# Kernel tuning notes

Measured on AMD Instinct MI355X. Metric: run time of the kernel, lower is better.

The kernel has to match this reference:

```python
import jax, jax.numpy as jnp
import numpy as np

EMBED_DIM = 1024
NUM_HEADS = 16
HEAD_DIM = EMBED_DIM // NUM_HEADS


def setup_inputs() -> dict:
    key = jax.random.key(0)
    ks = jax.random.split(key, 9)
    s = 1.0 / np.sqrt(EMBED_DIM)
    inp = {"x": jax.random.normal(ks[0], (2, 2048, EMBED_DIM), dtype=jnp.float32)}
    for i, name in enumerate(["q", "k", "v", "out"]):
        inp[f"W_{name}"] = jax.random.uniform(ks[1 + 2 * i], (EMBED_DIM, EMBED_DIM), jnp.float32, -s, s)
        inp[f"b_{name}"] = jax.random.uniform(ks[2 + 2 * i], (EMBED_DIM,), jnp.float32, -s, s)
    return inp


def _heads(x):
    # [B, S, D] -> [B, H, S, Dh]
    b, s, _ = x.shape
    return x.reshape(b, s, NUM_HEADS, HEAD_DIM).transpose(0, 2, 1, 3)


def reference(x, W_q, b_q, W_k, b_k, W_v, b_v, W_out, b_out):
    q = _heads(x @ W_q.T + b_q)
    k = _heads(x @ W_k.T + b_k)
    v = _heads(x @ W_v.T + b_v)
    scale = HEAD_DIM ** 0.5
    logits = jnp.einsum("bhqd,bhkd->bhqk", q, k) / scale  # [B,H,S,S]
    s = x.shape[1]
    causal = jnp.tril(jnp.ones((s, s), dtype=bool))
    logits = jnp.where(causal, logits, -jnp.inf)
    a = jax.nn.softmax(logits, axis=-1)
    o = jnp.einsum("bhqk,bhkd->bhqd", a, v)
    o = o.transpose(0, 2, 1, 3).reshape(x.shape[0], s, EMBED_DIM)
    return o @ W_out.T + b_out
```

## Files before the change

### kernel.cpp

```cpp
#include <hip/hip_runtime.h>
#include <hip/hip_bf16.h>

typedef __bf16 bf16_t;
typedef __bf16 bf16x8 __attribute__((ext_vector_type(8)));
typedef __bf16 bf16x4 __attribute__((ext_vector_type(4)));
typedef float  f32x4  __attribute__((ext_vector_type(4)));

#define MFMA16(a, b, c) __builtin_amdgcn_mfma_f32_16x16x32_bf16((a), (b), (c), 0, 0, 0)

constexpr int E  = 1024;
constexpr int S  = 2048;
constexpr int H  = 16;
constexpr int M  = 4096;

__device__ __forceinline__ void glds16(const bf16_t* src, bf16_t* dst) {
  __builtin_amdgcn_global_load_lds(
      (const __attribute__((address_space(1))) void*)src,
      (__attribute__((address_space(3))) void*)dst, 16, 0, 0);
}

template <int ROWS, int NT>
__device__ __forceinline__ void stage_tile(const bf16_t* g, int gld,
                                           bf16_t* lds, int tid) {
  const int w = tid >> 6, l = tid & 63;
#pragma unroll
  for (int i = 0; i < ROWS * 8 / NT; ++i) {
    const int c = i * NT + w * 64 + l;
    const int row = c >> 3;
    const int gch = (c & 7) ^ (row & 7);
    glds16(g + (size_t)row * gld + gch * 8, lds + (size_t)(i * NT + w * 64) * 8);
  }
}

__device__ __forceinline__ void stage_A_chunk(const bf16_t* g, int c,
                                              bf16_t* lds, int tid) {
  const int w = tid >> 6, l = tid & 63;
#pragma unroll
  for (int i = 0; i < 2; ++i) {
    const int gc = i * 512 + w * 64 + l;
    const int row_l = gc >> 3;
    const int col8 = gc & 7;
    const int h = row_l >> 6, rr = row_l & 63;
    const int row = h * 128 + c * 64 + rr;
    const int gch = col8 ^ (row & 7);
    glds16(g + (size_t)row * E + gch * 8, lds + ((size_t)row * 8 + col8) * 8);
  }
}

__device__ __forceinline__ bf16x8 read_frag(const bf16_t* lds, int row, int kc) {
  return *(const bf16x8*)(lds + (size_t)((row << 3) + (kc ^ (row & 7))) * 8);
}

__global__ void cvt_all_kernel(const float* __restrict__ x,
                               const float* __restrict__ w0, const float* __restrict__ w1,
                               const float* __restrict__ w2, const float* __restrict__ w3,
                               bf16_t* __restrict__ xb,
                               bf16_t* __restrict__ o0, bf16_t* __restrict__ o1,
                               bf16_t* __restrict__ o2, bf16_t* __restrict__ o3) {
  const int bid = blockIdx.x;
  const float* s;
  bf16_t* d;
  int idx;
  if (bid < 4096) {
    s = x; d = xb; idx = bid * 256 + threadIdx.x;
  } else {
    const int seg = (bid - 4096) >> 10;
    s = seg == 0 ? w0 : seg == 1 ? w1 : seg == 2 ? w2 : w3;
    d = seg == 0 ? o0 : seg == 1 ? o1 : seg == 2 ? o2 : o3;
    idx = ((bid - 4096) & 1023) * 256 + threadIdx.x;
  }
  float4 v = ((const float4*)s)[idx];
  bf16x4 o;
  o[0] = (bf16_t)v.x; o[1] = (bf16_t)v.y; o[2] = (bf16_t)v.z; o[3] = (bf16_t)v.w;
  ((bf16x4*)d)[idx] = o;
}

__global__ __launch_bounds__(512, 1) void qkv8_kernel(
    const bf16_t* __restrict__ xb, const bf16_t* __restrict__ W3,
    const float* __restrict__ bq, const float* __restrict__ bk,
    const float* __restrict__ bv, bf16_t* __restrict__ QKb,
    bf16_t* __restrict__ VT) {
  __shared__ __align__(16) bf16_t As[2][256 * 64];
  __shared__ __align__(16) bf16_t Bs[2][256 * 64];
  const int tid = threadIdx.x;
  const int l = tid & 63, lq = l & 15, qd = l >> 4;
  const int w = tid >> 6, wm = w >> 2, wn = w & 3;

  const int swz = (blockIdx.x & 7) * 24 + (blockIdx.x >> 3);
  const int by = swz / 12, bx = swz % 12;
  const int m0 = by * 256, n0 = bx * 256;

  const bf16_t* Ag = xb + (size_t)m0 * E;
  const bf16_t* Bg = W3 + (size_t)n0 * E;

  f32x4 acc[8][4];
#pragma unroll
  for (int jj = 0; jj < 8; ++jj)
#pragma unroll
    for (int n = 0; n < 4; ++n) acc[jj][n] = (f32x4){0.f, 0.f, 0.f, 0.f};

  stage_tile<128, 512>(Bg, E, Bs[0], tid);
  stage_tile<128, 512>(Bg + (size_t)128 * E, E, Bs[0] + 128 * 64, tid);
  stage_A_chunk(Ag, 0, As[0], tid);
  stage_A_chunk(Ag, 1, As[0], tid);
  asm volatile("s_waitcnt vmcnt(2)" ::: "memory");
  __builtin_amdgcn_s_barrier();

#pragma unroll 1
  for (int g = 0; g < 16; ++g) {
    const int s = g & 1;
    const bf16_t* Al = As[s];
    const bf16_t* Bl = Bs[s];
    bf16_t* An = As[s ^ 1];
    bf16_t* Bn = Bs[s ^ 1];
    const bf16_t* Agn = Ag + (g + 1) * 64;
    const bf16_t* Bgn = Bg + (g + 1) * 64;
    const bool more = (g < 15);
    bf16x8 af[4], bfr[4];

#pragma unroll
    for (int jj = 0; jj < 4; ++jj)
      af[jj] = read_frag(Al, wm * 128 + jj * 16 + lq, qd);
#pragma unroll
    for (int n = 0; n < 4; ++n)
      bfr[n] = read_frag(Bl, wn * 64 + n * 16 + lq, qd);
    if (more) stage_tile<128, 512>(Bgn, E, Bn, tid);
    __builtin_amdgcn_s_barrier();
    asm volatile("s_waitcnt lgkmcnt(0)" ::: "memory");
    __builtin_amdgcn_sched_barrier(0);
    __builtin_amdgcn_s_setprio(1);
#pragma unroll
    for (int jj = 0; jj < 4; ++jj)
#pragma unroll
      for (int n = 0; n < 4; ++n)
        acc[jj][n] = MFMA16(af[jj], bfr[n], acc[jj][n]);
    __builtin_amdgcn_s_setprio(0);
    if (more) asm volatile("s_waitcnt vmcnt(2)" ::: "memory");
    else      asm volatile("s_waitcnt vmcnt(0)" ::: "memory");
    __builtin_amdgcn_s_barrier();

#pragma unroll
    for (int jj = 0; jj < 4; ++jj)
      af[jj] = read_frag(Al, wm * 128 + (4 + jj) * 16 + lq, qd);
    if (more) stage_tile<128, 512>(Bgn + (size_t)128 * E, E, Bn + 128 * 64, tid);
    __builtin_amdgcn_s_barrier();
    asm volatile("s_waitcnt lgkmcnt(0)" ::: "memory");
    __builtin_amdgcn_sched_barrier(0);
    __builtin_amdgcn_s_setprio(1);
#pragma unroll
    for (int jj = 0; jj < 4; ++jj)
#pragma unroll
      for (int n = 0; n < 4; ++n)
        acc[4 + jj][n] = MFMA16(af[jj], bfr[n], acc[4 + jj][n]);
    __builtin_amdgcn_s_setprio(0);
    __builtin_amdgcn_s_barrier();

#pragma unroll
    for (int jj = 0; jj < 4; ++jj)
      af[jj] = read_frag(Al, wm * 128 + jj * 16 + lq, 4 + qd);
#pragma unroll
    for (int n = 0; n < 4; ++n)
      bfr[n] = read_frag(Bl, wn * 64 + n * 16 + lq, 4 + qd);
    if (more) stage_A_chunk(Agn, 0, An, tid);
    __builtin_amdgcn_s_barrier();
    asm volatile("s_waitcnt lgkmcnt(0)" ::: "memory");
    __builtin_amdgcn_sched_barrier(0);
    __builtin_amdgcn_s_setprio(1);
#pragma unroll
    for (int jj = 0; jj < 4; ++jj)
#pragma unroll
      for (int n = 0; n < 4; ++n)
        acc[jj][n] = MFMA16(af[jj], bfr[n], acc[jj][n]);
    __builtin_amdgcn_s_setprio(0);
    __builtin_amdgcn_s_barrier();

#pragma unroll
    for (int jj = 0; jj < 4; ++jj)
      af[jj] = read_frag(Al, wm * 128 + (4 + jj) * 16 + lq, 4 + qd);
    if (more) stage_A_chunk(Agn, 1, An, tid);
    __builtin_amdgcn_s_barrier();
    asm volatile("s_waitcnt lgkmcnt(0)" ::: "memory");
    __builtin_amdgcn_sched_barrier(0);
    __builtin_amdgcn_s_setprio(1);
#pragma unroll
    for (int jj = 0; jj < 4; ++jj)
#pragma unroll
      for (int n = 0; n < 4; ++n)
        acc[4 + jj][n] = MFMA16(af[jj], bfr[n], acc[4 + jj][n]);
    __builtin_amdgcn_s_setprio(0);
    if (more) asm volatile("s_waitcnt vmcnt(2)" ::: "memory");
    __builtin_amdgcn_s_barrier();
  }

  const int mat = n0 >> 10;
  const int ccb = n0 & 1023;
  const float* bp = (mat == 0) ? bq : (mat == 1) ? bk : bv;
  if (mat < 2) {
    const float sc = (mat == 0) ? 0.18033688011112043f : 1.0f;
    bf16_t* Out = QKb + (size_t)mat * ((size_t)M * E);
#pragma unroll
    for (int n = 0; n < 4; ++n) {
      const int cc = ccb + wn * 64 + n * 16 + lq;
      const float bvv = bp[cc];
#pragma unroll
      for (int jj = 0; jj < 8; ++jj)
#pragma unroll
        for (int r = 0; r < 4; ++r) {
          const int row = m0 + wm * 128 + jj * 16 + qd * 4 + r;
          Out[(size_t)row * E + cc] = (bf16_t)((acc[jj][n][r] + bvv) * sc);
        }
    }
  } else {
#pragma unroll
    for (int n = 0; n < 4; ++n) {
      const int cc = ccb + wn * 64 + n * 16 + lq;
      const float bvv = bp[cc];
      const int d = cc & 63, hh = cc >> 6;
#pragma unroll
      for (int jj = 0; jj < 8; ++jj) {
        const int row = m0 + wm * 128 + jj * 16 + qd * 4;
        const int bb_ = row >> 11;
        const int s_loc = row & (S - 1);
        const int sl = s_loc & 63, s0 = s_loc & ~63;
        const int a = sl >> 4, b4 = (sl >> 2) & 3;
        const int pb = (a >> 1) * 32 + b4 * 8 + (a & 1) * 4;
        bf16x4 vv;
#pragma unroll
        for (int r = 0; r < 4; ++r) vv[r] = (bf16_t)(acc[jj][n][r] + bvv);
        *(bf16x4*)&VT[((size_t)((bb_ * 16 + hh) * 64 + d)) * S + s0 + pb] = vv;
      }
    }
  }
}

__global__ __launch_bounds__(256) void oproj_gemm_kernel(
    const bf16_t* __restrict__ Ob, const bf16_t* __restrict__ wo,
    const float* __restrict__ bo, float* __restrict__ out) {
  __shared__ __align__(16) bf16_t As[64 * 64];
  __shared__ __align__(16) bf16_t Bs[128 * 64];
  const int tid = threadIdx.x;
  const int n0 = blockIdx.x * 128;
  const int m0 = blockIdx.y * 64;
  const int w = tid >> 6, l = tid & 63, lq = l & 15, qd = l >> 4;
  const int wr = (w >> 1) * 32, wc = (w & 1) * 64;

  f32x4 acc[2][4];
#pragma unroll
  for (int i = 0; i < 2; ++i)
#pragma unroll
    for (int j = 0; j < 4; ++j) acc[i][j] = (f32x4){0.f, 0.f, 0.f, 0.f};

  for (int kt = 0; kt < 16; ++kt) {
    __syncthreads();
    stage_tile<64, 256>(Ob + (size_t)m0 * E + kt * 64, E, As, tid);
    stage_tile<128, 256>(wo + (size_t)n0 * E + kt * 64, E, Bs, tid);
    __syncthreads();
#pragma unroll
    for (int ks = 0; ks < 2; ++ks) {
      bf16x8 af[2], bw[4];
#pragma unroll
      for (int mi = 0; mi < 2; ++mi)
        af[mi] = read_frag(As, wr + mi * 16 + lq, ks * 4 + qd);
#pragma unroll
      for (int ni = 0; ni < 4; ++ni)
        bw[ni] = read_frag(Bs, wc + ni * 16 + lq, ks * 4 + qd);
#pragma unroll
      for (int mi = 0; mi < 2; ++mi)
#pragma unroll
        for (int ni = 0; ni < 4; ++ni)
          acc[mi][ni] = MFMA16(af[mi], bw[ni], acc[mi][ni]);
    }
  }
#pragma unroll
  for (int ni = 0; ni < 4; ++ni) {
    const int col = n0 + wc + ni * 16 + lq;
    const float bvv = bo[col];
#pragma unroll
    for (int mi = 0; mi < 2; ++mi)
#pragma unroll
      for (int r = 0; r < 4; ++r) {
        const int row = m0 + wr + mi * 16 + qd * 4 + r;
        out[(size_t)row * E + col] = acc[mi][ni][r] + bvv;
      }
  }
}

__global__ __launch_bounds__(256, 2) void attn_kernel(
    const bf16_t* __restrict__ Q, const bf16_t* __restrict__ K,
    const bf16_t* __restrict__ VT, bf16_t* __restrict__ O) {
  __shared__ __align__(16) bf16_t Ks[2][64 * 64];
  __shared__ __align__(16) bf16_t Vt[3][64 * 64];

  const int tid = threadIdx.x;
  const int w = tid >> 6, l = tid & 63;
  const int lq = l & 15, qd = l >> 4;
  const int bid = blockIdx.x;
  const int g = bid & 7, t = bid >> 3;
  const int bh = g * 4 + (t & 3);
  const int p = t >> 2;
  const int b = bh >> 4, h = bh & 15;
  const size_t rowbase = (size_t)b * S;
  const bf16_t* Kg = K + rowbase * E + h * 64;
  const bf16_t* Vg = VT + (size_t)bh * 64 * S;

  bf16x8 ones;
#pragma unroll
  for (int j = 0; j < 8; ++j) ones[j] = (bf16_t)1.0f;

  stage_tile<64, 256>(Kg, E, Ks[0], tid);
  stage_tile<64, 256>(Vg, S, Vt[0], tid);
  int cb = 0;
  int vcur = 0;

#pragma unroll 1
  for (int seg = 0; seg < 2; ++seg) {
    const int qt = seg ? p : 31 - p;
    const int qr = qt * 64 + w * 16;

    bf16x8 aq[2];
#pragma unroll
    for (int ks = 0; ks < 2; ++ks)
      aq[ks] = *(const bf16x8*)(Q + (rowbase + qr + lq) * E + h * 64 +
                                ks * 32 + qd * 8);

    f32x4 oacc[4];
#pragma unroll
    for (int nt = 0; nt < 4; ++nt) oacc[nt] = (f32x4){0.f, 0.f, 0.f, 0.f};
    f32x4 osum = (f32x4){0.f, 0.f, 0.f, 0.f};
    bf16x8 ap_prev[2];
    int vprev = vcur;

    auto do_pv = [&](const bf16_t* Vp) {
#pragma unroll
      for (int ks = 0; ks < 2; ++ks) {
        bf16x8 bv[4];
#pragma unroll
        for (int nt = 0; nt < 4; ++nt)
          bv[nt] = read_frag(Vp, nt * 16 + lq, ks * 4 + qd);
#pragma unroll
        for (int nt = 0; nt < 4; ++nt)
          oacc[nt] = MFMA16(ap_prev[ks], bv[nt], oacc[nt]);
        osum = MFMA16(ap_prev[ks], ones, osum);
      }
    };

    for (int kt = 0; kt <= qt; ++kt) {
      __syncthreads();
      const int vnext = (vcur + 1 == 3) ? 0 : vcur + 1;
      if (kt < qt) {
        const int kn = (kt + 1) * 64;
        stage_tile<64, 256>(Kg + (size_t)kn * E, E, Ks[cb ^ 1], tid);
        stage_tile<64, 256>(Vg + kn, S, Vt[vnext], tid);
      } else if (seg == 0) {
        stage_tile<64, 256>(Kg, E, Ks[cb ^ 1], tid);
        stage_tile<64, 256>(Vg, S, Vt[vnext], tid);
      }
      const bf16_t* Kc = Ks[cb];
      const int k0 = kt * 64;
      const bool needmask = (kt == qt);

      f32x4 sacc[4];
#pragma unroll
      for (int nt = 0; nt < 4; ++nt) sacc[nt] = (f32x4){0.f, 0.f, 0.f, 0.f};
      __builtin_amdgcn_s_setprio(1);
#pragma unroll
      for (int ks = 0; ks < 2; ++ks) {
        bf16x8 bk[4];
#pragma unroll
        for (int nt = 0; nt < 4; ++nt)
          bk[nt] = read_frag(Kc, nt * 16 + lq, ks * 4 + qd);
#pragma unroll
        for (int nt = 0; nt < 4; ++nt)
          sacc[nt] = MFMA16(bk[nt], aq[ks], sacc[nt]);
      }
      if (kt > 0) do_pv(Vt[vprev]);
      __builtin_amdgcn_s_setprio(0);

#pragma unroll
      for (int nt = 0; nt < 4; ++nt)
#pragma unroll
        for (int r = 0; r < 4; ++r) {
          float pv = __builtin_amdgcn_exp2f(sacc[nt][r]);
          if (needmask) {
            const int kg = k0 + nt * 16 + qd * 4 + r;
            const int qg = qr + lq;
            pv = (kg > qg) ? 0.f : pv;
          }
          ap_prev[nt >> 1][((nt & 1) << 2) | r] = (bf16_t)pv;
        }
      vprev = vcur;
      vcur = vnext;
      cb ^= 1;
    }
    do_pv(Vt[vprev]);

    float rinv[4];
#pragma unroll
    for (int r = 0; r < 4; ++r) rinv[r] = 1.0f / osum[r];
#pragma unroll
    for (int nt = 0; nt < 4; ++nt)
#pragma unroll
      for (int r = 0; r < 4; ++r) {
        const int qg = qr + qd * 4 + r;
        O[(rowbase + qg) * E + h * 64 + nt * 16 + lq] =
            (bf16_t)(oacc[nt][r] * rinv[r]);
      }
  }
}

extern "C" void kernel_launch(void* const* d_in, const int* in_sizes, int n_in,
                              void* d_out, int out_size, void* d_ws, size_t ws_size,
                              hipStream_t stream) {
  const float* x  = (const float*)d_in[0];
  const float* Wq = (const float*)d_in[1];
  const float* bq = (const float*)d_in[2];
  const float* Wk = (const float*)d_in[3];
  const float* bk = (const float*)d_in[4];
  const float* Wv = (const float*)d_in[5];
  const float* bv = (const float*)d_in[6];
  const float* Wo = (const float*)d_in[7];
  const float* bo = (const float*)d_in[8];
  float* out = (float*)d_out;

  unsigned char* ws = (unsigned char*)d_ws;
  constexpr size_t MB = 1ull << 20;
  bf16_t* xb  = (bf16_t*)(ws + 0 * MB);
  bf16_t* wqb = (bf16_t*)(ws + 8 * MB);
  bf16_t* wkb = (bf16_t*)(ws + 10 * MB);
  bf16_t* wvb = (bf16_t*)(ws + 12 * MB);
  bf16_t* wob = (bf16_t*)(ws + 14 * MB);
  bf16_t* Qb  = (bf16_t*)(ws + 16 * MB);
  bf16_t* VT  = (bf16_t*)(ws + 40 * MB);
  bf16_t* Ob  = xb;

  cvt_all_kernel<<<4096 + 4 * 1024, 256, 0, stream>>>(
      x, Wq, Wk, Wv, Wo, xb, wqb, wkb, wvb, wob);

  qkv8_kernel<<<192, 512, 0, stream>>>(xb, wqb, bq, bk, bv, Qb, VT);

  attn_kernel<<<512, 256, 0, stream>>>(Qb, Qb + (size_t)M * E, VT, Ob);

  oproj_gemm_kernel<<<dim3(8, 64), 256, 0, stream>>>(Ob, wob, bo, out);
}
```

Measured before the change: 174.1 us.

## Use 128-key tiles in attention and compute row sums with VALU shuffles

The attention kernel now processes 128 keys per iteration instead of 64, with double-buffered K and V tiles and a new 128-wide V staging and swizzle. The softmax denominator is accumulated on the vector ALUs and reduced across lanes with shuffles, replacing the extra MFMA against a ones vector. The one-iteration software pipeline of the PV product is removed. Fewer barriers and larger MFMA batches per iteration are gained, at the cost of more LDS use, more registers, and masked work on the diagonal tile growing to 128 keys.

```diff
diff --git a/kernel.cpp b/kernel.cpp
--- a/kernel.cpp
+++ b/kernel.cpp
@@ -29,6 +29,17 @@
     const int row = c >> 3;
     const int gch = (c & 7) ^ (row & 7);
     glds16(g + (size_t)row * gld + gch * 8, lds + (size_t)(i * NT + w * 64) * 8);
+  }
+}
+
+__device__ __forceinline__ void stage_v128(const bf16_t* g, int gld,
+                                           bf16_t* lds, int tid) {
+#pragma unroll
+  for (int i = 0; i < 4; ++i) {
+    const int c = i * 256 + tid;
+    const int row = c >> 4, col16 = c & 15;
+    const int gch = col16 ^ (row & 7);
+    glds16(g + (size_t)row * gld + gch * 8, lds + (size_t)c * 8);
   }
 }
 
@@ -49,6 +60,10 @@
 
 __device__ __forceinline__ bf16x8 read_frag(const bf16_t* lds, int row, int kc) {
   return *(const bf16x8*)(lds + (size_t)((row << 3) + (kc ^ (row & 7))) * 8);
+}
+
+__device__ __forceinline__ bf16x8 read_v128(const bf16_t* lds, int row, int kc) {
+  return *(const bf16x8*)(lds + (size_t)((row << 4) + (kc ^ (row & 7))) * 8);
 }
 
 __global__ void cvt_all_kernel(const float* __restrict__ x,
@@ -288,8 +303,8 @@
 __global__ __launch_bounds__(256, 2) void attn_kernel(
     const bf16_t* __restrict__ Q, const bf16_t* __restrict__ K,
     const bf16_t* __restrict__ VT, bf16_t* __restrict__ O) {
-  __shared__ __align__(16) bf16_t Ks[2][64 * 64];
-  __shared__ __align__(16) bf16_t Vt[3][64 * 64];
+  __shared__ __align__(16) bf16_t Ks[2][128 * 64];
+  __shared__ __align__(16) bf16_t Vt[2][64 * 128];
 
   const int tid = threadIdx.x;
   const int w = tid >> 6, l = tid & 63;
@@ -303,19 +318,16 @@
   const bf16_t* Kg = K + rowbase * E + h * 64;
   const bf16_t* Vg = VT + (size_t)bh * 64 * S;
 
-  bf16x8 ones;
-#pragma unroll
-  for (int j = 0; j < 8; ++j) ones[j] = (bf16_t)1.0f;
-
-  stage_tile<64, 256>(Kg, E, Ks[0], tid);
-  stage_tile<64, 256>(Vg, S, Vt[0], tid);
+  stage_tile<128, 256>(Kg, E, Ks[0], tid);
+  stage_v128(Vg, S, Vt[0], tid);
   int cb = 0;
-  int vcur = 0;
 
 #pragma unroll 1
   for (int seg = 0; seg < 2; ++seg) {
     const int qt = seg ? p : 31 - p;
+    const int T = (qt + 2) >> 1;
     const int qr = qt * 64 + w * 16;
+    const int qg = qr + lq;
 
     bf16x8 aq[2];
 #pragma unroll
@@ -326,83 +338,89 @@
     f32x4 oacc[4];
 #pragma unroll
     for (int nt = 0; nt < 4; ++nt) oacc[nt] = (f32x4){0.f, 0.f, 0.f, 0.f};
-    f32x4 osum = (f32x4){0.f, 0.f, 0.f, 0.f};
-    bf16x8 ap_prev[2];
-    int vprev = vcur;
-
-    auto do_pv = [&](const bf16_t* Vp) {
+    float rs4[4] = {0.f, 0.f, 0.f, 0.f};
+
+    for (int kt = 0; kt < T; ++kt) {
+      __syncthreads();
+      if (kt < T - 1) {
+        const int kn = (kt + 1) * 128;
+        stage_tile<128, 256>(Kg + (size_t)kn * E, E, Ks[cb ^ 1], tid);
+        stage_v128(Vg + kn, S, Vt[cb ^ 1], tid);
+      } else if (seg == 0) {
+        stage_tile<128, 256>(Kg, E, Ks[cb ^ 1], tid);
+        stage_v128(Vg, S, Vt[cb ^ 1], tid);
+      }
+      const bf16_t* Kc = Ks[cb];
+      const bf16_t* Vc = Vt[cb];
+      const int k0 = kt * 128;
+      const bool needmask = (kt == T - 1);
+
+      f32x4 sacc[8];
+#pragma unroll
+      for (int nt = 0; nt < 8; ++nt) sacc[nt] = (f32x4){0.f, 0.f, 0.f, 0.f};
+      __builtin_amdgcn_s_setprio(1);
 #pragma unroll
       for (int ks = 0; ks < 2; ++ks) {
+        bf16x8 bk[8];
+#pragma unroll
+        for (int nt = 0; nt < 8; ++nt)
+          bk[nt] = read_frag(Kc, nt * 16 + lq, ks * 4 + qd);
+#pragma unroll
+        for (int nt = 0; nt < 8; ++nt)
+          sacc[nt] = MFMA16(bk[nt], aq[ks], sacc[nt]);
+      }
+      __builtin_amdgcn_s_setprio(0);
+
+      bf16x8 ap[4];
+      if (needmask) {
+#pragma unroll
+        for (int nt = 0; nt < 8; ++nt)
+#pragma unroll
+          for (int r = 0; r < 4; ++r) {
+            float pv = __builtin_amdgcn_exp2f(sacc[nt][r]);
+            const int kg = k0 + nt * 16 + qd * 4 + r;
+            pv = (kg > qg) ? 0.f : pv;
+            rs4[nt & 3] += pv;
+            ap[nt >> 1][((nt & 1) << 2) | r] = (bf16_t)pv;
+          }
+      } else {
+#pragma unroll
+        for (int nt = 0; nt < 8; ++nt)
+#pragma unroll
+          for (int r = 0; r < 4; ++r) {
+            float pv = __builtin_amdgcn_exp2f(sacc[nt][r]);
+            rs4[nt & 3] += pv;
+            ap[nt >> 1][((nt & 1) << 2) | r] = (bf16_t)pv;
+          }
+      }
+
+      __builtin_amdgcn_s_setprio(1);
+#pragma unroll
+      for (int c = 0; c < 4; ++c) {
         bf16x8 bv[4];
 #pragma unroll
         for (int nt = 0; nt < 4; ++nt)
-          bv[nt] = read_frag(Vp, nt * 16 + lq, ks * 4 + qd);
+          bv[nt] = read_v128(Vc, nt * 16 + lq, c * 4 + qd);
 #pragma unroll
         for (int nt = 0; nt < 4; ++nt)
-          oacc[nt] = MFMA16(ap_prev[ks], bv[nt], oacc[nt]);
-        osum = MFMA16(ap_prev[ks], ones, osum);
-      }
-    };
-
-    for (int kt = 0; kt <= qt; ++kt) {
-      __syncthreads();
-      const int vnext = (vcur + 1 == 3) ? 0 : vcur + 1;
-      if (kt < qt) {
-        const int kn = (kt + 1) * 64;
-        stage_tile<64, 256>(Kg + (size_t)kn * E, E, Ks[cb ^ 1], tid);
-        stage_tile<64, 256>(Vg + kn, S, Vt[vnext], tid);
-      } else if (seg == 0) {
-        stage_tile<64, 256>(Kg, E, Ks[cb ^ 1], tid);
-        stage_tile<64, 256>(Vg, S, Vt[vnext], tid);
-      }
-      const bf16_t* Kc = Ks[cb];
-      const int k0 = kt * 64;
-      const bool needmask = (kt == qt);
-
-      f32x4 sacc[4];
-#pragma unroll
-      for (int nt = 0; nt < 4; ++nt) sacc[nt] = (f32x4){0.f, 0.f, 0.f, 0.f};
-      __builtin_amdgcn_s_setprio(1);
-#pragma unroll
-      for (int ks = 0; ks < 2; ++ks) {
-        bf16x8 bk[4];
-#pragma unroll
-        for (int nt = 0; nt < 4; ++nt)
-          bk[nt] = read_frag(Kc, nt * 16 + lq, ks * 4 + qd);
-#pragma unroll
-        for (int nt = 0; nt < 4; ++nt)
-          sacc[nt] = MFMA16(bk[nt], aq[ks], sacc[nt]);
-      }
-      if (kt > 0) do_pv(Vt[vprev]);
+          oacc[nt] = MFMA16(ap[c], bv[nt], oacc[nt]);
+      }
       __builtin_amdgcn_s_setprio(0);
-
-#pragma unroll
-      for (int nt = 0; nt < 4; ++nt)
-#pragma unroll
-        for (int r = 0; r < 4; ++r) {
-          float pv = __builtin_amdgcn_exp2f(sacc[nt][r]);
-          if (needmask) {
-            const int kg = k0 + nt * 16 + qd * 4 + r;
-            const int qg = qr + lq;
-            pv = (kg > qg) ? 0.f : pv;
-          }
-          ap_prev[nt >> 1][((nt & 1) << 2) | r] = (bf16_t)pv;
-        }
-      vprev = vcur;
-      vcur = vnext;
       cb ^= 1;
     }
-    do_pv(Vt[vprev]);
-
+
+    float rs = (rs4[0] + rs4[1]) + (rs4[2] + rs4[3]);
+    rs += __shfl_xor(rs, 16);
+    rs += __shfl_xor(rs, 32);
     float rinv[4];
 #pragma unroll
-    for (int r = 0; r < 4; ++r) rinv[r] = 1.0f / osum[r];
+    for (int r = 0; r < 4; ++r) rinv[r] = 1.0f / __shfl(rs, qd * 4 + r);
 #pragma unroll
     for (int nt = 0; nt < 4; ++nt)
 #pragma unroll
       for (int r = 0; r < 4; ++r) {
-        const int qg = qr + qd * 4 + r;
-        O[(rowbase + qg) * E + h * 64 + nt * 16 + lq] =
+        const int qgw = qr + qd * 4 + r;
+        O[(rowbase + qgw) * E + h * 64 + nt * 16 + lq] =
             (bf16_t)(oacc[nt][r] * rinv[r]);
       }
   }
```

Result: no change. 173.8 us (-0.2%).
